# Performance work log

Hardware: AMD Instinct MI355X
Metric: run time of the kernel (lower is better)

The kernel has to match this reference:

```python
import jax, jax.numpy as jnp
import numpy as np

N = 100000
E = 1600000
IN_C, HID_C, OUT_C = 64, 64, 40

def setup_inputs() -> dict:
    key = jax.random.key(0)
    ks = jax.random.split(key, 12)
    x = jax.random.normal(ks[0], (N, IN_C), dtype=jnp.float32)
    edge_index = jax.random.randint(ks[1], (2, E), 0, N, dtype=jnp.int32)
    def glorot(k, fan_in, fan_out):
        lim = float(np.sqrt(6.0 / (fan_in + fan_out)))
        return jax.random.uniform(k, (fan_in, fan_out), jnp.float32, -lim, lim)
    return {
        "x": x,
        "edge_index": edge_index,
        "W0_0": glorot(ks[2], IN_C, HID_C), "W1_0": glorot(ks[3], IN_C, HID_C), "b_0": jnp.zeros((HID_C,), jnp.float32),
        "W0_1": glorot(ks[4], HID_C, HID_C), "W1_1": glorot(ks[5], HID_C, HID_C), "b_1": jnp.zeros((HID_C,), jnp.float32),
        "W0_2": glorot(ks[6], HID_C, OUT_C), "W1_2": glorot(ks[7], HID_C, OUT_C), "b_2": jnp.zeros((OUT_C,), jnp.float32),
    }

def _cheb_norm(edge_index, num_nodes, dtype):
    # PyG ChebConv.__norm__ with normalization=None, edge_weight=None -> ones.
    # L = D - A; lambda_max = 2 * max(L weights); scaled: 2L/lambda_max - I.
    src, dst = edge_index[0], edge_index[1]
    w = jnp.ones((edge_index.shape[1],), dtype)
    deg = jax.ops.segment_sum(w, src, num_segments=num_nodes)
    lam = 2.0 * jnp.maximum(jnp.max(deg), jnp.max(-w))
    scale = 2.0 / lam
    norm_edge = -w * scale            # off-diagonal entries
    norm_loop = deg * scale - 1.0     # diagonal entries (self-loop mask subtracts 1)
    return norm_edge, norm_loop

def _spmm(x, src, dst, norm_edge, norm_loop, num_nodes):
    # y[i] = sum_{e: src->i} norm_e * x[src_e] + norm_loop[i] * x[i]
    msg = norm_edge[:, None] * x[src]
    return jax.ops.segment_sum(msg, dst, num_segments=num_nodes) + norm_loop[:, None] * x

def reference(x, edge_index, W0_0, W1_0, b_0, W0_1, W1_1, b_1, W0_2, W1_2, b_2):
    num_nodes = x.shape[0]
    src, dst = edge_index[0], edge_index[1]
    norm_edge, norm_loop = _cheb_norm(edge_index, num_nodes, x.dtype)

    def cheb(h, W0, W1, b):
        # K=2: out = T0(L) h W0 + T1(L) h W1 + b, T0 = I, T1 = scaled L
        Tx1 = _spmm(h, src, dst, norm_edge, norm_loop, num_nodes)
        return h @ W0 + Tx1 @ W1 + b

    h = jax.nn.relu(cheb(x, W0_0, W1_0, b_0))   # dropout is identity in eval mode
    h = jax.nn.relu(cheb(h, W0_1, W1_1, b_1))
    h = cheb(h, W0_2, W1_2, b_2)
    return jax.nn.log_softmax(h, axis=-1)
```

## Files before the change

kernel.cpp:

```cpp
#include <hip/hip_runtime.h>
#include <math.h>

#define N_NODES 100000
#define N_EDGES 1600000
#define OUTC 40
#define PAIRS40 20

#define NC 32
#define CHUNK (N_EDGES / NC)

#define RANGE_H 65536
#define NR_H 2
#define NPAD_H (NR_H * RANGE_H)

#define RANGE_F 32768
#define NR_F 4

#define SCAN_BLOCK 1024
#define SCAN_NBLK ((N_NODES + SCAN_BLOCK - 1) / SCAN_BLOCK)

typedef float vf2 __attribute__((ext_vector_type(2)));
typedef __fp16 f16x2 __attribute__((ext_vector_type(2)));

__device__ inline unsigned pack_bf16x2(float lo, float hi) {
    unsigned a = __float_as_uint(lo), b = __float_as_uint(hi);
    a = (a + 0x7fffu + ((a >> 16) & 1u)) >> 16;
    b = (b + 0x7fffu + ((b >> 16) & 1u)) & 0xffff0000u;
    return a | b;
}
__device__ inline float bf_lo(unsigned u) { return __uint_as_float(u << 16); }
__device__ inline float bf_hi(unsigned u) { return __uint_as_float(u & 0xffff0000u); }

__device__ inline unsigned pk16(float a, float b) {
    f16x2 h = __builtin_amdgcn_cvt_pkrtz(a, b);
    return __builtin_bit_cast(unsigned, h);
}
__device__ inline f16x2 uph(unsigned u) { return __builtin_bit_cast(f16x2, u); }

__device__ inline float fdot2(f16x2 a, f16x2 b, float c) {
#if __has_builtin(__builtin_amdgcn_fdot2)
    return __builtin_amdgcn_fdot2(a, b, c, false);
#else
    float d;
    asm volatile("v_dot2_f32_f16 %0, %1, %2, %3" : "=v"(d) : "v"(a), "v"(b), "v"(c));
    return d;
#endif
}

__global__ __launch_bounds__(1024) void k_hist(const int* __restrict__ src,
                                               const int* __restrict__ dst,
                                               unsigned short* __restrict__ Hs,
                                               unsigned short* __restrict__ Hd) {
    __shared__ unsigned h32[RANGE_H / 2];
    int c = blockIdx.x, r = blockIdx.y;
    const int* a = blockIdx.z ? dst : src;
    unsigned short* H = blockIdx.z ? Hd : Hs;
    for (int k = threadIdx.x; k < RANGE_H / 2; k += 1024) h32[k] = 0;
    __syncthreads();
    int r0 = r * RANGE_H;
    int e0 = c * CHUNK, e1 = e0 + CHUNK;
    for (int e = e0 + threadIdx.x; e < e1; e += 1024) {
        unsigned d = (unsigned)(a[e] - r0);
        if (d < RANGE_H) atomicAdd(&h32[d >> 1], 1u << ((d & 1) * 16));
    }
    __syncthreads();
    for (int k = threadIdx.x; k < RANGE_H; k += 1024)
        H[c * NPAD_H + r0 + k] = (unsigned short)((h32[k >> 1] >> ((k & 1) * 16)) & 0xffffu);
}

__global__ __launch_bounds__(SCAN_BLOCK) void k_scan1(const unsigned short* __restrict__ Hs,
                                                      const unsigned short* __restrict__ Hd,
                                                      int* __restrict__ rowptr,
                                                      int* __restrict__ blocksum,
                                                      int* __restrict__ deg_src,
                                                      int* __restrict__ maxdeg) {
    __shared__ int buf[2][SCAN_BLOCK];
    int t = threadIdx.x;
    int i = blockIdx.x * SCAN_BLOCK + t;
    int vs = 0, vd = 0;
    if (i < N_NODES) {
        #pragma unroll
        for (int c = 0; c < NC; c++) { vs += Hs[c * NPAD_H + i]; vd += Hd[c * NPAD_H + i]; }
        deg_src[i] = vs;
    }
    int m = vs;
    for (int off = 32; off; off >>= 1) m = max(m, __shfl_down(m, off));
    if ((t & 63) == 0) atomicMax(maxdeg, m);
    int pd = (vd + 7) & ~7;
    int cur = 0;
    buf[0][t] = pd;
    __syncthreads();
    for (int off = 1; off < SCAN_BLOCK; off <<= 1) {
        int nv = buf[cur][t];
        if (t >= off) nv += buf[cur][t - off];
        buf[1 - cur][t] = nv;
        cur = 1 - cur;
        __syncthreads();
    }
    int incl = buf[cur][t];
    if (i < N_NODES) rowptr[i + 1] = incl;
    if (t == SCAN_BLOCK - 1) blocksum[blockIdx.x] = incl;
}

__global__ __launch_bounds__(SCAN_BLOCK) void k_finalize(const int* __restrict__ blocksum,
                                                         int* __restrict__ rowptr,
                                                         const unsigned short* __restrict__ Hd,
                                                         int* __restrict__ Bd,
                                                         int* __restrict__ csr_src) {
    __shared__ int soff;
    int t = threadIdx.x, blk = blockIdx.x;
    if (t == 0) {
        int r = 0;
        for (int j = 0; j < blk; j++) r += blocksum[j];
        soff = r;
        if (blk == 0) rowptr[0] = 0;
    }
    __syncthreads();
    int i = blk * SCAN_BLOCK + t;
    if (i >= N_NODES) return;
    int tmp[NC];
    int s = 0;
    #pragma unroll
    for (int c = 0; c < NC; c++) { tmp[c] = Hd[c * NPAD_H + i]; s += tmp[c]; }
    int rf = rowptr[i + 1] + soff;
    rowptr[i + 1] = rf;
    int pd = (s + 7) & ~7;
    int run = rf - pd;
    #pragma unroll
    for (int c = 0; c < NC; c++) { Bd[c * NPAD_H + i] = run; run += tmp[c]; }
    for (int k = run; k < rf; k++) csr_src[k] = N_NODES;
}

__global__ __launch_bounds__(1024) void k_fill2(const int* __restrict__ src,
                                                const int* __restrict__ dst,
                                                const int* __restrict__ basepos,
                                                int* __restrict__ csr_src) {
    __shared__ int pos[RANGE_F];
    int c = blockIdx.x, r = blockIdx.y;
    int r0 = r * RANGE_F;
    for (int k = threadIdx.x; k < RANGE_F; k += 1024) pos[k] = basepos[c * NPAD_H + r0 + k];
    __syncthreads();
    int e0 = c * CHUNK, e1 = e0 + CHUNK;
    for (int e = e0 + threadIdx.x; e < e1; e += 1024) {
        unsigned d = (unsigned)(dst[e] - r0);
        if (d < RANGE_F) {
            int s = src[e];
            int p = atomicAdd(&pos[d], 1);
            csr_src[p] = s;
        }
    }
}

__global__ __launch_bounds__(256, 8) void k_gemm64(const float* __restrict__ hf,
                                                   const float* __restrict__ W0,
                                                   const float* __restrict__ W1,
                                                   const float* __restrict__ b,
                                                   const int* __restrict__ deg_src,
                                                   const int* __restrict__ maxdeg,
                                                   unsigned* __restrict__ G0b,
                                                   unsigned short* __restrict__ G1f8) {
    __shared__ uint4 swu[32 * 32];
    __shared__ unsigned shu[32 * 32];
    int t = threadIdx.x;
    const float2* W02 = (const float2*)W0;
    const float2* W12 = (const float2*)W1;
    for (int cell = t; cell < 1024; cell += 256) {
        int kp = cell >> 5, c2 = cell & 31;
        float2 a  = W02[(kp * 2) * 32 + c2];
        float2 bb = W02[(kp * 2 + 1) * 32 + c2];
        float2 cc = W12[(kp * 2) * 32 + c2];
        float2 dd = W12[(kp * 2 + 1) * 32 + c2];
        swu[cell] = make_uint4(pk16(a.x, bb.x), pk16(a.y, bb.y), pk16(cc.x, dd.x), pk16(cc.y, dd.y));
    }
    int i0 = blockIdx.x * 32;
    const float4* h4 = (const float4*)(hf + (size_t)i0 * 64);
    {
        float4 f0 = h4[t * 2], f1 = h4[t * 2 + 1];
        ((uint4*)shu)[t] = make_uint4(pk16(f0.x, f0.y), pk16(f0.z, f0.w), pk16(f1.x, f1.y), pk16(f1.z, f1.w));
    }
    if (blockIdx.x == 0 && t < 16) ((unsigned*)G1f8)[N_NODES * 16 + t] = 0;
    __syncthreads();
    int c2 = t & 31, rg = t >> 5;
    float scale = 1.0f / (float)(*maxdeg);
    float2 b2 = ((const float2*)b)[c2];
    float a0x[4], a0y[4], a1x[4], a1y[4];
    #pragma unroll
    for (int p = 0; p < 4; p++) { a0x[p] = b2.x; a0y[p] = b2.y; a1x[p] = 0.f; a1y[p] = 0.f; }
    #pragma unroll 8
    for (int kp = 0; kp < 32; kp++) {
        uint4 w = swu[kp * 32 + c2];
        f16x2 w0x = uph(w.x), w0y = uph(w.y), w1x = uph(w.z), w1y = uph(w.w);
        #pragma unroll
        for (int p = 0; p < 4; p++) {
            f16x2 h2 = uph(shu[(rg + 8 * p) * 32 + kp]);
            a0x[p] = fdot2(h2, w0x, a0x[p]);
            a0y[p] = fdot2(h2, w0y, a0y[p]);
            a1x[p] = fdot2(h2, w1x, a1x[p]);
            a1y[p] = fdot2(h2, w1y, a1y[p]);
        }
    }
    #pragma unroll
    for (int p = 0; p < 4; p++) {
        int row = i0 + rg + 8 * p;
        float nl = (float)deg_src[row] * scale - 1.0f;
        G0b[row * 32 + c2] = pack_bf16x2(a0x[p] + nl * a1x[p], a0y[p] + nl * a1y[p]);
        int pk = __builtin_amdgcn_cvt_pk_fp8_f32(a1x[p], a1y[p], 0, false);
        G1f8[row * 32 + c2] = (unsigned short)(pk & 0xffff);
    }
}

__global__ __launch_bounds__(256, 6) void k_fs64_g64(const unsigned* __restrict__ G0b_in,
                                                     const unsigned char* __restrict__ g1_in,
                                                     const int* __restrict__ rowptr,
                                                     const int* __restrict__ csr_src,
                                                     const int* __restrict__ deg_src,
                                                     const int* __restrict__ maxdeg,
                                                     const float* __restrict__ W0,
                                                     const float* __restrict__ W1,
                                                     const float* __restrict__ b,
                                                     unsigned* __restrict__ G0b_out,
                                                     unsigned short* __restrict__ G1f8_out) {
    __shared__ uint4 swu[32 * 32];
    __shared__ unsigned shu[32 * 32];
    int t = threadIdx.x;
    const float2* W02 = (const float2*)W0;
    const float2* W12 = (const float2*)W1;
    for (int cell = t; cell < 1024; cell += 256) {
        int kp = cell >> 5, c2 = cell & 31;
        float2 a  = W02[(kp * 2) * 32 + c2];
        float2 bb = W02[(kp * 2 + 1) * 32 + c2];
        float2 cc = W12[(kp * 2) * 32 + c2];
        float2 dd = W12[(kp * 2 + 1) * 32 + c2];
        swu[cell] = make_uint4(pk16(a.x, bb.x), pk16(a.y, bb.y), pk16(cc.x, dd.x), pk16(cc.y, dd.y));
    }
    int waveId = t >> 6, lane = t & 63;
    int ch = lane & 7;
    int local = waveId * 8 + (lane >> 3);
    int node = blockIdx.x * 32 + local;
    float scale = 1.0f / (float)(*maxdeg);
    int e0 = rowptr[node], e1 = rowptr[node + 1];
    int octbase = lane & 56;
    vf2 acc[4];
    acc[0] = 0.f; acc[1] = 0.f; acc[2] = 0.f; acc[3] = 0.f;
    uint2 u[8];
    int idxB = 0;
    int e = e0;
    if (e < e1) {
        int idxA = csr_src[e + ch];
        if (e + 8 < e1) idxB = csr_src[e + 8 + ch];
        #pragma unroll
        for (int j = 0; j < 8; j++) {
            int s = __shfl(idxA, octbase | j);
            u[j] = ((const uint2*)(g1_in + (size_t)s * 64))[ch];
        }
    }
    while (e < e1) {
        int en = e + 8;
        int idxC = 0;
        if (en + 8 < e1) idxC = csr_src[en + 8 + ch];
        uint2 n[8];
        if (en < e1) {
            #pragma unroll
            for (int j = 0; j < 8; j++) {
                int s = __shfl(idxB, octbase | j);
                n[j] = ((const uint2*)(g1_in + (size_t)s * 64))[ch];
            }
        }
        #pragma unroll
        for (int j = 0; j < 8; j++) {
            acc[0] += __builtin_amdgcn_cvt_pk_f32_fp8((int)u[j].x, false);
            acc[1] += __builtin_amdgcn_cvt_pk_f32_fp8((int)u[j].x, true);
            acc[2] += __builtin_amdgcn_cvt_pk_f32_fp8((int)u[j].y, false);
            acc[3] += __builtin_amdgcn_cvt_pk_f32_fp8((int)u[j].y, true);
        }
        #pragma unroll
        for (int j = 0; j < 8; j++) u[j] = n[j];
        idxB = idxC;
        e = en;
    }
    uint4 g = ((const uint4*)(G0b_in + (size_t)node * 32))[ch];
    float v0 = fmaxf(bf_lo(g.x) - scale * acc[0].x, 0.f);
    float v1 = fmaxf(bf_hi(g.x) - scale * acc[0].y, 0.f);
    float v2 = fmaxf(bf_lo(g.y) - scale * acc[1].x, 0.f);
    float v3 = fmaxf(bf_hi(g.y) - scale * acc[1].y, 0.f);
    float v4 = fmaxf(bf_lo(g.z) - scale * acc[2].x, 0.f);
    float v5 = fmaxf(bf_hi(g.z) - scale * acc[2].y, 0.f);
    float v6 = fmaxf(bf_lo(g.w) - scale * acc[3].x, 0.f);
    float v7 = fmaxf(bf_hi(g.w) - scale * acc[3].y, 0.f);
    ((uint4*)shu)[local * 8 + ch] = make_uint4(pk16(v0, v1), pk16(v2, v3), pk16(v4, v5), pk16(v6, v7));
    if (blockIdx.x == 0 && t < 16) ((unsigned*)G1f8_out)[N_NODES * 16 + t] = 0;
    __syncthreads();
    int c2 = t & 31, rg = t >> 5;
    int i0 = blockIdx.x * 32;
    float2 b2 = ((const float2*)b)[c2];
    float a0x[4], a0y[4], a1x[4], a1y[4];
    #pragma unroll
    for (int p = 0; p < 4; p++) { a0x[p] = b2.x; a0y[p] = b2.y; a1x[p] = 0.f; a1y[p] = 0.f; }
    #pragma unroll 8
    for (int kp = 0; kp < 32; kp++) {
        uint4 w = swu[kp * 32 + c2];
        f16x2 w0x = uph(w.x), w0y = uph(w.y), w1x = uph(w.z), w1y = uph(w.w);
        #pragma unroll
        for (int p = 0; p < 4; p++) {
            f16x2 h2 = uph(shu[(rg + 8 * p) * 32 + kp]);
            a0x[p] = fdot2(h2, w0x, a0x[p]);
            a0y[p] = fdot2(h2, w0y, a0y[p]);
            a1x[p] = fdot2(h2, w1x, a1x[p]);
            a1y[p] = fdot2(h2, w1y, a1y[p]);
        }
    }
    #pragma unroll
    for (int p = 0; p < 4; p++) {
        int row = i0 + rg + 8 * p;
        float nl = (float)deg_src[row] * scale - 1.0f;
        G0b_out[row * 32 + c2] = pack_bf16x2(a0x[p] + nl * a1x[p], a0y[p] + nl * a1y[p]);
        int pk = __builtin_amdgcn_cvt_pk_fp8_f32(a1x[p], a1y[p], 0, false);
        G1f8_out[row * 32 + c2] = (unsigned short)(pk & 0xffff);
    }
}

__global__ __launch_bounds__(256, 6) void k_fs64_g40(const unsigned* __restrict__ G0b_in,
                                                     const unsigned char* __restrict__ g1_in,
                                                     const int* __restrict__ rowptr,
                                                     const int* __restrict__ csr_src,
                                                     const int* __restrict__ deg_src,
                                                     const int* __restrict__ maxdeg,
                                                     const float* __restrict__ W0,
                                                     const float* __restrict__ W1,
                                                     const float* __restrict__ b,
                                                     unsigned* __restrict__ G0b_out,
                                                     unsigned short* __restrict__ G1f8_out) {
    __shared__ uint4 swu[32 * PAIRS40];
    __shared__ unsigned shu[32 * 32];
    int t = threadIdx.x;
    const float2* W02 = (const float2*)W0;
    const float2* W12 = (const float2*)W1;
    for (int cell = t; cell < 32 * PAIRS40; cell += 256) {
        int kp = cell / PAIRS40, c2 = cell % PAIRS40;
        float2 a  = W02[(kp * 2) * PAIRS40 + c2];
        float2 bb = W02[(kp * 2 + 1) * PAIRS40 + c2];
        float2 cc = W12[(kp * 2) * PAIRS40 + c2];
        float2 dd = W12[(kp * 2 + 1) * PAIRS40 + c2];
        swu[cell] = make_uint4(pk16(a.x, bb.x), pk16(a.y, bb.y), pk16(cc.x, dd.x), pk16(cc.y, dd.y));
    }
    int waveId = t >> 6, lane = t & 63;
    int ch = lane & 7;
    int local = waveId * 8 + (lane >> 3);
    int node = blockIdx.x * 32 + local;
    float scale = 1.0f / (float)(*maxdeg);
    int e0 = rowptr[node], e1 = rowptr[node + 1];
    int octbase = lane & 56;
    vf2 acc[4];
    acc[0] = 0.f; acc[1] = 0.f; acc[2] = 0.f; acc[3] = 0.f;
    uint2 u[8];
    int idxB = 0;
    int e = e0;
    if (e < e1) {
        int idxA = csr_src[e + ch];
        if (e + 8 < e1) idxB = csr_src[e + 8 + ch];
        #pragma unroll
        for (int j = 0; j < 8; j++) {
            int s = __shfl(idxA, octbase | j);
            u[j] = ((const uint2*)(g1_in + (size_t)s * 64))[ch];
        }
    }
    while (e < e1) {
        int en = e + 8;
        int idxC = 0;
        if (en + 8 < e1) idxC = csr_src[en + 8 + ch];
        uint2 n[8];
        if (en < e1) {
            #pragma unroll
            for (int j = 0; j < 8; j++) {
                int s = __shfl(idxB, octbase | j);
                n[j] = ((const uint2*)(g1_in + (size_t)s * 64))[ch];
            }
        }
        #pragma unroll
        for (int j = 0; j < 8; j++) {
            acc[0] += __builtin_amdgcn_cvt_pk_f32_fp8((int)u[j].x, false);
            acc[1] += __builtin_amdgcn_cvt_pk_f32_fp8((int)u[j].x, true);
            acc[2] += __builtin_amdgcn_cvt_pk_f32_fp8((int)u[j].y, false);
            acc[3] += __builtin_amdgcn_cvt_pk_f32_fp8((int)u[j].y, true);
        }
        #pragma unroll
        for (int j = 0; j < 8; j++) u[j] = n[j];
        idxB = idxC;
        e = en;
    }
    uint4 g = ((const uint4*)(G0b_in + (size_t)node * 32))[ch];
    float v0 = fmaxf(bf_lo(g.x) - scale * acc[0].x, 0.f);
    float v1 = fmaxf(bf_hi(g.x) - scale * acc[0].y, 0.f);
    float v2 = fmaxf(bf_lo(g.y) - scale * acc[1].x, 0.f);
    float v3 = fmaxf(bf_hi(g.y) - scale * acc[1].y, 0.f);
    float v4 = fmaxf(bf_lo(g.z) - scale * acc[2].x, 0.f);
    float v5 = fmaxf(bf_hi(g.z) - scale * acc[2].y, 0.f);
    float v6 = fmaxf(bf_lo(g.w) - scale * acc[3].x, 0.f);
    float v7 = fmaxf(bf_hi(g.w) - scale * acc[3].y, 0.f);
    ((uint4*)shu)[local * 8 + ch] = make_uint4(pk16(v0, v1), pk16(v2, v3), pk16(v4, v5), pk16(v6, v7));
    if (blockIdx.x == 0 && t < 10) ((unsigned*)G1f8_out)[N_NODES * 10 + t] = 0;
    __syncthreads();
    int c2 = t & 31, rg = t >> 5;
    if (c2 >= PAIRS40) return;
    int i0 = blockIdx.x * 32;
    float2 b2 = ((const float2*)b)[c2];
    float a0x[4], a0y[4], a1x[4], a1y[4];
    #pragma unroll
    for (int p = 0; p < 4; p++) { a0x[p] = b2.x; a0y[p] = b2.y; a1x[p] = 0.f; a1y[p] = 0.f; }
    #pragma unroll 8
    for (int kp = 0; kp < 32; kp++) {
        uint4 w = swu[kp * PAIRS40 + c2];
        f16x2 w0x = uph(w.x), w0y = uph(w.y), w1x = uph(w.z), w1y = uph(w.w);
        #pragma unroll
        for (int p = 0; p < 4; p++) {
            f16x2 h2 = uph(shu[(rg + 8 * p) * 32 + kp]);
            a0x[p] = fdot2(h2, w0x, a0x[p]);
            a0y[p] = fdot2(h2, w0y, a0y[p]);
            a1x[p] = fdot2(h2, w1x, a1x[p]);
            a1y[p] = fdot2(h2, w1y, a1y[p]);
        }
    }
    #pragma unroll
    for (int p = 0; p < 4; p++) {
        int row = i0 + rg + 8 * p;
        float nl = (float)deg_src[row] * scale - 1.0f;
        G0b_out[row * PAIRS40 + c2] = pack_bf16x2(a0x[p] + nl * a1x[p], a0y[p] + nl * a1y[p]);
        int pk = __builtin_amdgcn_cvt_pk_fp8_f32(a1x[p], a1y[p], 0, false);
        G1f8_out[row * PAIRS40 + c2] = (unsigned short)(pk & 0xffff);
    }
}

__global__ __launch_bounds__(256, 6) void k_spmm40(const unsigned* __restrict__ G0b,
                                                   const unsigned char* __restrict__ g1,
                                                   const int* __restrict__ rowptr,
                                                   const int* __restrict__ csr_src,
                                                   const int* __restrict__ maxdeg,
                                                   float* __restrict__ out) {
    int t = threadIdx.x;
    int waveId = t >> 6, lane = t & 63;
    int ch = lane & 7;
    bool act = ch < 5;
    int node = blockIdx.x * 32 + waveId * 8 + (lane >> 3);
    float scale = 1.0f / (float)(*maxdeg);
    int e0 = rowptr[node], e1 = rowptr[node + 1];
    int octbase = lane & 56;
    vf2 acc[4];
    acc[0] = 0.f; acc[1] = 0.f; acc[2] = 0.f; acc[3] = 0.f;
    uint2 u[8];
    int idxB = 0;
    int e = e0;
    if (e < e1) {
        int idxA = csr_src[e + ch];
        if (e + 8 < e1) idxB = csr_src[e + 8 + ch];
        #pragma unroll
        for (int j = 0; j < 8; j++) {
            int s = __shfl(idxA, octbase | j);
            if (act) u[j] = ((const uint2*)(g1 + (size_t)s * 40))[ch];
        }
    }
    while (e < e1) {
        int en = e + 8;
        int idxC = 0;
        if (en + 8 < e1) idxC = csr_src[en + 8 + ch];
        uint2 n[8];
        if (en < e1) {
            #pragma unroll
            for (int j = 0; j < 8; j++) {
                int s = __shfl(idxB, octbase | j);
                if (act) n[j] = ((const uint2*)(g1 + (size_t)s * 40))[ch];
            }
        }
        if (act) {
            #pragma unroll
            for (int j = 0; j < 8; j++) {
                acc[0] += __builtin_amdgcn_cvt_pk_f32_fp8((int)u[j].x, false);
                acc[1] += __builtin_amdgcn_cvt_pk_f32_fp8((int)u[j].x, true);
                acc[2] += __builtin_amdgcn_cvt_pk_f32_fp8((int)u[j].y, false);
                acc[3] += __builtin_amdgcn_cvt_pk_f32_fp8((int)u[j].y, true);
            }
        }
        #pragma unroll
        for (int j = 0; j < 8; j++) u[j] = n[j];
        idxB = idxC;
        e = en;
    }
    float v[8];
    float m = -INFINITY;
    if (act) {
        uint4 g = ((const uint4*)(G0b + (size_t)node * PAIRS40))[ch];
        v[0] = bf_lo(g.x) - scale * acc[0].x;
        v[1] = bf_hi(g.x) - scale * acc[0].y;
        v[2] = bf_lo(g.y) - scale * acc[1].x;
        v[3] = bf_hi(g.y) - scale * acc[1].y;
        v[4] = bf_lo(g.z) - scale * acc[2].x;
        v[5] = bf_hi(g.z) - scale * acc[2].y;
        v[6] = bf_lo(g.w) - scale * acc[3].x;
        v[7] = bf_hi(g.w) - scale * acc[3].y;
        #pragma unroll
        for (int q = 0; q < 8; q++) m = fmaxf(m, v[q]);
    }
    m = fmaxf(m, __shfl_xor(m, 1));
    m = fmaxf(m, __shfl_xor(m, 2));
    m = fmaxf(m, __shfl_xor(m, 4));
    float s = 0.f;
    if (act) {
        #pragma unroll
        for (int q = 0; q < 8; q++) s += __expf(v[q] - m);
    }
    s += __shfl_xor(s, 1);
    s += __shfl_xor(s, 2);
    s += __shfl_xor(s, 4);
    float ls = __logf(s);
    if (act) {
        float4 oA, oB;
        oA.x = v[0] - m - ls; oA.y = v[1] - m - ls; oA.z = v[2] - m - ls; oA.w = v[3] - m - ls;
        oB.x = v[4] - m - ls; oB.y = v[5] - m - ls; oB.z = v[6] - m - ls; oB.w = v[7] - m - ls;
        float4* o4 = (float4*)(out + (size_t)node * 40);
        o4[ch * 2] = oA;
        o4[ch * 2 + 1] = oB;
    }
}


extern "C" void kernel_launch(void* const* d_in, const int* in_sizes, int n_in,
                              void* d_out, int out_size, void* d_ws, size_t ws_size,
                              hipStream_t stream) {
    const float* x   = (const float*)d_in[0];
    const int* ei    = (const int*)d_in[1];
    const int* src   = ei;
    const int* dst   = ei + N_EDGES;
    const float* W0_0 = (const float*)d_in[2];
    const float* W1_0 = (const float*)d_in[3];
    const float* b_0  = (const float*)d_in[4];
    const float* W0_1 = (const float*)d_in[5];
    const float* W1_1 = (const float*)d_in[6];
    const float* b_1  = (const float*)d_in[7];
    const float* W0_2 = (const float*)d_in[8];
    const float* W1_2 = (const float*)d_in[9];
    const float* b_2  = (const float*)d_in[10];
    float* outp = (float*)d_out;

    int* ip = (int*)d_ws;
    int* deg_src  = ip;
    int* rowptr   = ip + 100000;
    int* blocksum = ip + 200064;
    int* maxdeg   = ip + 200192;
    int* csr_src  = ip + 200256;
    unsigned short* Hs = (unsigned short*)(ip + 2700256);
    unsigned short* Hd = (unsigned short*)(ip + 4797408);
    int* Bd       = ip + 6894560;
    unsigned* GA0 = (unsigned*)(ip + 11088864);
    unsigned short* GA1 = (unsigned short*)(ip + 14288864);
    unsigned* GB0 = (unsigned*)(ip + 15888928);
    unsigned short* GB1 = (unsigned short*)(ip + 19088928);

    (void)hipMemsetAsync(maxdeg, 0, sizeof(int), stream);

    k_hist<<<dim3(NC, NR_H, 2), 1024, 0, stream>>>(src, dst, Hs, Hd);
    k_scan1<<<SCAN_NBLK, SCAN_BLOCK, 0, stream>>>(Hs, Hd, rowptr, blocksum, deg_src, maxdeg);
    k_finalize<<<SCAN_NBLK, SCAN_BLOCK, 0, stream>>>(blocksum, rowptr, Hd, Bd, csr_src);
    k_fill2<<<dim3(NC, NR_F), 1024, 0, stream>>>(src, dst, Bd, csr_src);

    const int GS = N_NODES / 32;

    k_gemm64<<<GS, 256, 0, stream>>>(x, W0_0, W1_0, b_0, deg_src, maxdeg, GA0, GA1);
    k_fs64_g64<<<GS, 256, 0, stream>>>(GA0, (const unsigned char*)GA1, rowptr, csr_src,
                                       deg_src, maxdeg, W0_1, W1_1, b_1, GB0, GB1);
    k_fs64_g40<<<GS, 256, 0, stream>>>(GB0, (const unsigned char*)GB1, rowptr, csr_src,
                                       deg_src, maxdeg, W0_2, W1_2, b_2, GA0, GA1);
    k_spmm40<<<GS, 256, 0, stream>>>(GA0, (const unsigned char*)GA1, rowptr, csr_src, maxdeg, outp);
}
```

Baseline: 300.2 us.

## Fuse CSR fill and first-layer GEMM into one launch with smaller ranges

```diff
diff --git a/kernel.cpp b/kernel.cpp
--- a/kernel.cpp
+++ b/kernel.cpp
@@ -9,12 +9,16 @@
 #define NC 32
 #define CHUNK (N_EDGES / NC)
 
-#define RANGE_H 65536
-#define NR_H 2
+#define RANGE_H 32768
+#define NR_H 4
 #define NPAD_H (NR_H * RANGE_H)
 
-#define RANGE_F 32768
-#define NR_F 4
+#define RANGE_F 16384
+#define NR_F 7
+
+#define FILLB (NC * NR_F)
+#define NB32 (N_NODES / 32)
+#define GEMB ((NB32 + 3) / 4)
 
 #define SCAN_BLOCK 1024
 #define SCAN_NBLK ((N_NODES + SCAN_BLOCK - 1) / SCAN_BLOCK)
@@ -131,56 +135,65 @@
     for (int k = run; k < rf; k++) csr_src[k] = N_NODES;
 }
 
-__global__ __launch_bounds__(1024) void k_fill2(const int* __restrict__ src,
-                                                const int* __restrict__ dst,
-                                                const int* __restrict__ basepos,
-                                                int* __restrict__ csr_src) {
-    __shared__ int pos[RANGE_F];
-    int c = blockIdx.x, r = blockIdx.y;
-    int r0 = r * RANGE_F;
-    for (int k = threadIdx.x; k < RANGE_F; k += 1024) pos[k] = basepos[c * NPAD_H + r0 + k];
-    __syncthreads();
-    int e0 = c * CHUNK, e1 = e0 + CHUNK;
-    for (int e = e0 + threadIdx.x; e < e1; e += 1024) {
-        unsigned d = (unsigned)(dst[e] - r0);
-        if (d < RANGE_F) {
-            int s = src[e];
-            int p = atomicAdd(&pos[d], 1);
-            csr_src[p] = s;
-        }
-    }
-}
-
-__global__ __launch_bounds__(256, 8) void k_gemm64(const float* __restrict__ hf,
-                                                   const float* __restrict__ W0,
-                                                   const float* __restrict__ W1,
-                                                   const float* __restrict__ b,
-                                                   const int* __restrict__ deg_src,
-                                                   const int* __restrict__ maxdeg,
-                                                   unsigned* __restrict__ G0b,
-                                                   unsigned short* __restrict__ G1f8) {
-    __shared__ uint4 swu[32 * 32];
-    __shared__ unsigned shu[32 * 32];
+__global__ __launch_bounds__(1024) void k_fill_gemm(const int* __restrict__ src,
+                                                    const int* __restrict__ dst,
+                                                    const int* __restrict__ basepos,
+                                                    int* __restrict__ csr_src,
+                                                    const float* __restrict__ hf,
+                                                    const float* __restrict__ W0,
+                                                    const float* __restrict__ W1,
+                                                    const float* __restrict__ b,
+                                                    const int* __restrict__ deg_src,
+                                                    const int* __restrict__ maxdeg,
+                                                    unsigned* __restrict__ G0b,
+                                                    unsigned short* __restrict__ G1f8) {
+    __shared__ union {
+        int pos[RANGE_F];
+        struct { uint4 swu[32 * 32]; unsigned shu[4 * 1024]; } g;
+    } sm;
     int t = threadIdx.x;
+    if (blockIdx.x < FILLB) {
+        int c = blockIdx.x / NR_F, r = blockIdx.x % NR_F;
+        int r0 = r * RANGE_F;
+        for (int k = t; k < RANGE_F; k += 1024) sm.pos[k] = basepos[c * NPAD_H + r0 + k];
+        __syncthreads();
+        int e0 = c * CHUNK, e1 = e0 + CHUNK;
+        for (int e = e0 + t; e < e1; e += 1024) {
+            unsigned d = (unsigned)(dst[e] - r0);
+            if (d < RANGE_F) {
+                int s = src[e];
+                int p = atomicAdd(&sm.pos[d], 1);
+                csr_src[p] = s;
+            }
+        }
+        return;
+    }
+    int gb = blockIdx.x - FILLB;
+    int sub = t >> 8, tt = t & 255;
+    int nb = gb * 4 + sub;
+    bool ok = nb < NB32;
     const float2* W02 = (const float2*)W0;
     const float2* W12 = (const float2*)W1;
-    for (int cell = t; cell < 1024; cell += 256) {
-        int kp = cell >> 5, c2 = cell & 31;
+    {
+        int kp = t >> 5, c2 = t & 31;
         float2 a  = W02[(kp * 2) * 32 + c2];
         float2 bb = W02[(kp * 2 + 1) * 32 + c2];
         float2 cc = W12[(kp * 2) * 32 + c2];
         float2 dd = W12[(kp * 2 + 1) * 32 + c2];
-        swu[cell] = make_uint4(pk16(a.x, bb.x), pk16(a.y, bb.y), pk16(cc.x, dd.x), pk16(cc.y, dd.y));
-    }
-    int i0 = blockIdx.x * 32;
-    const float4* h4 = (const float4*)(hf + (size_t)i0 * 64);
-    {
-        float4 f0 = h4[t * 2], f1 = h4[t * 2 + 1];
-        ((uint4*)shu)[t] = make_uint4(pk16(f0.x, f0.y), pk16(f0.z, f0.w), pk16(f1.x, f1.y), pk16(f1.z, f1.w));
-    }
-    if (blockIdx.x == 0 && t < 16) ((unsigned*)G1f8)[N_NODES * 16 + t] = 0;
-    __syncthreads();
-    int c2 = t & 31, rg = t >> 5;
+        sm.g.swu[t] = make_uint4(pk16(a.x, bb.x), pk16(a.y, bb.y), pk16(cc.x, dd.x), pk16(cc.y, dd.y));
+    }
+    if (ok) {
+        const float4* h4 = (const float4*)(hf + (size_t)(nb * 32) * 64);
+        float4 f0 = h4[tt * 2], f1 = h4[tt * 2 + 1];
+        ((uint4*)(sm.g.shu + sub * 1024))[tt] =
+            make_uint4(pk16(f0.x, f0.y), pk16(f0.z, f0.w), pk16(f1.x, f1.y), pk16(f1.z, f1.w));
+    }
+    if (blockIdx.x == FILLB && t < 16) ((unsigned*)G1f8)[N_NODES * 16 + t] = 0;
+    __syncthreads();
+    if (!ok) return;
+    int c2 = tt & 31, rg = tt >> 5;
+    int i0 = nb * 32;
+    const unsigned* shu = sm.g.shu + sub * 1024;
     float scale = 1.0f / (float)(*maxdeg);
     float2 b2 = ((const float2*)b)[c2];
     float a0x[4], a0y[4], a1x[4], a1y[4];
@@ -188,7 +201,7 @@
     for (int p = 0; p < 4; p++) { a0x[p] = b2.x; a0y[p] = b2.y; a1x[p] = 0.f; a1y[p] = 0.f; }
     #pragma unroll 8
     for (int kp = 0; kp < 32; kp++) {
-        uint4 w = swu[kp * 32 + c2];
+        uint4 w = sm.g.swu[kp * 32 + c2];
         f16x2 w0x = uph(w.x), w0y = uph(w.y), w1x = uph(w.z), w1y = uph(w.w);
         #pragma unroll
         for (int p = 0; p < 4; p++) {
@@ -559,11 +572,12 @@
     k_hist<<<dim3(NC, NR_H, 2), 1024, 0, stream>>>(src, dst, Hs, Hd);
     k_scan1<<<SCAN_NBLK, SCAN_BLOCK, 0, stream>>>(Hs, Hd, rowptr, blocksum, deg_src, maxdeg);
     k_finalize<<<SCAN_NBLK, SCAN_BLOCK, 0, stream>>>(blocksum, rowptr, Hd, Bd, csr_src);
-    k_fill2<<<dim3(NC, NR_F), 1024, 0, stream>>>(src, dst, Bd, csr_src);
+
+    k_fill_gemm<<<FILLB + GEMB, 1024, 0, stream>>>(src, dst, Bd, csr_src,
+                                                   x, W0_0, W1_0, b_0, deg_src, maxdeg, GA0, GA1);
 
     const int GS = N_NODES / 32;
 
-    k_gemm64<<<GS, 256, 0, stream>>>(x, W0_0, W1_0, b_0, deg_src, maxdeg, GA0, GA1);
     k_fs64_g64<<<GS, 256, 0, stream>>>(GA0, (const unsigned char*)GA1, rowptr, csr_src,
                                        deg_src, maxdeg, W0_1, W1_1, b_1, GB0, GB1);
     k_fs64_g40<<<GS, 256, 0, stream>>>(GB0, (const unsigned char*)GB1, rowptr, csr_src,
```

After: 301.4 us. About the same (+0.4%).
